# Performance work log

Measured on AMD Instinct MI355X. Metric: run time of the kernel, lower is better.

Reference implementation:

```python
import jax, jax.numpy as jnp
import numpy as np

B, V, D = 4096, 10000, 512
ANNEAL = 1.0
EPSILON = 1.0  # regularization_type = 'OT'


def setup_inputs() -> dict:
    key = jax.random.key(0)
    ks = jax.random.split(key, 8)
    return {
        "recon_x": jax.random.normal(ks[0], (B, V), dtype=jnp.float32),
        "logits_rec": jax.random.normal(ks[1], (B, V), dtype=jnp.float32),
        "logits_text": jax.random.normal(ks[2], (B, V), dtype=jnp.float32),
        "x": jax.random.uniform(ks[3], (B, V), dtype=jnp.float32),
        "mu": jax.random.normal(ks[4], (B, D), dtype=jnp.float32),
        "logvar": jax.random.normal(ks[5], (B, D), dtype=jnp.float32),
        "prior_mu": jax.random.normal(ks[6], (B, D), dtype=jnp.float32),
        "prior_logvar": jax.random.normal(ks[7], (B, D), dtype=jnp.float32),
    }


def _bce(logits, x):
    # -mean_b(mean_v(log_softmax(logits,1) * x)) == global mean since both
    # reductions are plain means over the full [B, V] tensor.
    return -jnp.mean(jax.nn.log_softmax(logits, axis=1) * x)


def _kld(m, lv):
    return -0.5 * jnp.mean(1.0 + lv - m * m - jnp.exp(lv))


def reference(recon_x, logits_rec, logits_text, x, mu, logvar, prior_mu, prior_logvar):
    BCE_merged = _bce(recon_x, x)
    BCE_text = _bce(logits_text, x)
    BCE_rec = _bce(logits_rec, x)
    BCE = (BCE_merged + BCE_text + BCE_rec) / 3.0

    KLD1 = _kld(mu, logvar)
    KLD2 = _kld(prior_mu, prior_logvar)

    # Bures-Wasserstein^2 between diagonal Gaussians. The torch code builds
    # dense diag matrices and runs batched Cholesky/bmm; for diagonal covs
    # L1 = diag(sqrt(s1)), L1 @ C2 @ L1^T = diag(s1*s2), chol -> diag(sqrt(s1*s2)),
    # so the math reduces exactly to the O(d) closed form below.
    s1 = jnp.exp(logvar)          # [B, D]
    s2 = jnp.exp(prior_logvar)    # [B, D]
    mean_dist_sq = jnp.sum((mu - prior_mu) ** 2, axis=1)            # [B]
    trace_term = jnp.sum(s1 + s2 - 2.0 * jnp.sqrt(s1 * s2), axis=1)  # [B]
    wasserstein_loss = jnp.mean(mean_dist_sq + trace_term)

    l = BCE + ANNEAL / 2.0 * (KLD1 + KLD2) + EPSILON * wasserstein_loss
    return (l, BCE, wasserstein_loss, BCE_rec, BCE_text, BCE_merged)
```

## Files before the change

### kernel.cpp

```cpp
#include <hip/hip_runtime.h>

#define NROWS 4096
#define NCOLS 10000
#define DDIM  512
#define NKLD  256

__device__ __forceinline__ float wave_reduce_sum(float v) {
    #pragma unroll
    for (int o = 32; o > 0; o >>= 1) v += __shfl_down(v, o, 64);
    return v;
}

__global__ __launch_bounds__(256) void fused_main_kernel(
    const float4* __restrict__ merged,
    const float4* __restrict__ rec,
    const float4* __restrict__ text,
    const float4* __restrict__ xr,
    const float4* __restrict__ mu, const float4* __restrict__ lv,
    const float4* __restrict__ pmu, const float4* __restrict__ plv,
    float* __restrict__ cm, float* __restrict__ ct, float* __restrict__ cr,
    float* __restrict__ k1o, float* __restrict__ k2o, float* __restrict__ wo)
{
    const int wave = threadIdx.x >> 6;
    const int lane = threadIdx.x & 63;

    if (blockIdx.x < NKLD) {
        const int nvec = NROWS * DDIM / 4;
        float k1 = 0.f, k2 = 0.f, wacc = 0.f;

        for (int i = blockIdx.x * 256 + threadIdx.x; i < nvec; i += NKLD * 256) {
            const float4 m  = mu[i];
            const float4 l  = lv[i];
            const float4 pm = pmu[i];
            const float4 pl = plv[i];

            #define KW_COMP(c)                                              \
            {                                                               \
                const float e1 = __expf(l.c);                               \
                const float e2 = __expf(pl.c);                              \
                k1 += 1.f + l.c - m.c * m.c - e1;                           \
                k2 += 1.f + pl.c - pm.c * pm.c - e2;                        \
                const float dm = m.c - pm.c;                                \
                wacc += dm * dm + e1 + e2 - 2.f * __expf(0.5f * (l.c + pl.c)); \
            }
            KW_COMP(x) KW_COMP(y) KW_COMP(z) KW_COMP(w)
            #undef KW_COMP
        }

        __shared__ float sm[4][3];
        k1 = wave_reduce_sum(k1);
        k2 = wave_reduce_sum(k2);
        wacc = wave_reduce_sum(wacc);
        if (lane == 0) { sm[wave][0] = k1; sm[wave][1] = k2; sm[wave][2] = wacc; }
        __syncthreads();
        if (threadIdx.x == 0) {
            k1o[blockIdx.x] = sm[0][0] + sm[1][0] + sm[2][0] + sm[3][0];
            k2o[blockIdx.x] = sm[0][1] + sm[1][1] + sm[2][1] + sm[3][1];
            wo[blockIdx.x]  = sm[0][2] + sm[1][2] + sm[2][2] + sm[3][2];
        }
        return;
    }

    const int row = blockIdx.x - NKLD;
    const int nvec = NCOLS / 4;
    const size_t base = (size_t)row * nvec;

    float se_m = 0.f, se_t = 0.f, se_r = 0.f;
    float d_m = 0.f, d_t = 0.f, d_r = 0.f;
    float sx = 0.f;

    #define BCE_BODY(xv, mv, tv, rv)                                          \
    {                                                                         \
        se_m += __expf(mv.x) + __expf(mv.y) + __expf(mv.z) + __expf(mv.w);    \
        se_t += __expf(tv.x) + __expf(tv.y) + __expf(tv.z) + __expf(tv.w);    \
        se_r += __expf(rv.x) + __expf(rv.y) + __expf(rv.z) + __expf(rv.w);    \
        d_m += mv.x * xv.x + mv.y * xv.y + mv.z * xv.z + mv.w * xv.w;         \
        d_t += tv.x * xv.x + tv.y * xv.y + tv.z * xv.z + tv.w * xv.w;         \
        d_r += rv.x * xv.x + rv.y * xv.y + rv.z * xv.z + rv.w * xv.w;         \
        sx  += xv.x + xv.y + xv.z + xv.w;                                     \
    }

    int i = threadIdx.x;
    for (; i + 256 < nvec; i += 512) {
        const float4 xv0 = xr[base + i];
        const float4 mv0 = merged[base + i];
        const float4 tv0 = text[base + i];
        const float4 rv0 = rec[base + i];
        const float4 xv1 = xr[base + i + 256];
        const float4 mv1 = merged[base + i + 256];
        const float4 tv1 = text[base + i + 256];
        const float4 rv1 = rec[base + i + 256];
        BCE_BODY(xv0, mv0, tv0, rv0)
        BCE_BODY(xv1, mv1, tv1, rv1)
    }
    for (; i < nvec; i += 256) {
        const float4 xv = xr[base + i];
        const float4 mv = merged[base + i];
        const float4 tv = text[base + i];
        const float4 rv = rec[base + i];
        BCE_BODY(xv, mv, tv, rv)
    }
    #undef BCE_BODY

    __shared__ float sm2[4][7];
    float vals[7] = {se_m, se_t, se_r, d_m, d_t, d_r, sx};
    #pragma unroll
    for (int k = 0; k < 7; ++k) vals[k] = wave_reduce_sum(vals[k]);
    if (lane == 0) {
        #pragma unroll
        for (int k = 0; k < 7; ++k) sm2[wave][k] = vals[k];
    }
    __syncthreads();

    if (threadIdx.x == 0) {
        float t[7];
        #pragma unroll
        for (int k = 0; k < 7; ++k)
            t[k] = sm2[0][k] + sm2[1][k] + sm2[2][k] + sm2[3][k];
        const float sumx = t[6];
        cm[row] = t[3] - __logf(t[0]) * sumx;
        ct[row] = t[4] - __logf(t[1]) * sumx;
        cr[row] = t[5] - __logf(t[2]) * sumx;
    }
}

__global__ __launch_bounds__(256) void finalize_kernel(
    const float* __restrict__ cm, const float* __restrict__ ct,
    const float* __restrict__ cr, const float* __restrict__ k1p,
    const float* __restrict__ k2p, const float* __restrict__ wp,
    float* __restrict__ out)
{
    float sm_ = 0.f, st_ = 0.f, sr_ = 0.f;
    for (int i = threadIdx.x; i < NROWS; i += 256) {
        sm_ += cm[i]; st_ += ct[i]; sr_ += cr[i];
    }
    float s1 = 0.f, s2 = 0.f, sw = 0.f;
    for (int i = threadIdx.x; i < NKLD; i += 256) {
        s1 += k1p[i]; s2 += k2p[i]; sw += wp[i];
    }

    __shared__ float sh[4][6];
    float vals[6] = {sm_, st_, sr_, s1, s2, sw};
    #pragma unroll
    for (int k = 0; k < 6; ++k) vals[k] = wave_reduce_sum(vals[k]);
    const int wave = threadIdx.x >> 6;
    const int lane = threadIdx.x & 63;
    if (lane == 0) {
        #pragma unroll
        for (int k = 0; k < 6; ++k) sh[wave][k] = vals[k];
    }
    __syncthreads();

    if (threadIdx.x == 0) {
        float t[6];
        #pragma unroll
        for (int k = 0; k < 6; ++k)
            t[k] = sh[0][k] + sh[1][k] + sh[2][k] + sh[3][k];

        const float invBV = 1.f / ((float)NROWS * (float)NCOLS);
        const float BCE_merged = -t[0] * invBV;
        const float BCE_text   = -t[1] * invBV;
        const float BCE_rec    = -t[2] * invBV;
        const float BCE = (BCE_merged + BCE_text + BCE_rec) * (1.f / 3.f);

        const float invBD = 1.f / ((float)NROWS * (float)DDIM);
        const float KLD1 = -0.5f * t[3] * invBD;
        const float KLD2 = -0.5f * t[4] * invBD;
        const float wass = t[5] / (float)NROWS;

        const float l = BCE + 0.5f * (KLD1 + KLD2) + wass;

        out[0] = l;
        out[1] = BCE;
        out[2] = wass;
        out[3] = BCE_rec;
        out[4] = BCE_text;
        out[5] = BCE_merged;
    }
}

extern "C" void kernel_launch(void* const* d_in, const int* in_sizes, int n_in,
                              void* d_out, int out_size, void* d_ws, size_t ws_size,
                              hipStream_t stream) {
    const float4* recon_x      = (const float4*)d_in[0];
    const float4* logits_rec   = (const float4*)d_in[1];
    const float4* logits_text  = (const float4*)d_in[2];
    const float4* x            = (const float4*)d_in[3];
    const float4* mu           = (const float4*)d_in[4];
    const float4* logvar       = (const float4*)d_in[5];
    const float4* prior_mu     = (const float4*)d_in[6];
    const float4* prior_logvar = (const float4*)d_in[7];

    float* ws = (float*)d_ws;
    float* cm = ws;
    float* ct = ws + NROWS;
    float* cr = ws + 2 * NROWS;
    float* k1p = ws + 3 * NROWS;
    float* k2p = ws + 3 * NROWS + NKLD;
    float* wp  = ws + 3 * NROWS + 2 * NKLD;

    hipLaunchKernelGGL(fused_main_kernel, dim3(NKLD + NROWS), dim3(256), 0, stream,
                       recon_x, logits_rec, logits_text, x,
                       mu, logvar, prior_mu, prior_logvar,
                       cm, ct, cr, k1p, k2p, wp);
    hipLaunchKernelGGL(finalize_kernel, dim3(1), dim3(256), 0, stream,
                       cm, ct, cr, k1p, k2p, wp, (float*)d_out);
}
```

Before: 128.9 us.

## Merge KLD/Wasserstein work into BCE row blocks, two rows per block

Removes the separate group of KLD blocks and hands each of 2048 blocks one float4 slice of the latent tensors plus two BCE rows, so every block is uniform. The BCE loop is unrolled three-deep instead of two to keep more loads in flight. The finalize kernel now reduces 2048 partials per quantity. Each block gets longer and there is an extra sync between rows, and the grid is smaller, which changes tail behaviour.

```diff
diff --git a/kernel.cpp b/kernel.cpp
--- a/kernel.cpp
+++ b/kernel.cpp
@@ -3,7 +3,7 @@
 #define NROWS 4096
 #define NCOLS 10000
 #define DDIM  512
-#define NKLD  256
+#define NBLK  2048
 
 __device__ __forceinline__ float wave_reduce_sum(float v) {
     #pragma unroll
@@ -24,103 +24,115 @@
     const int wave = threadIdx.x >> 6;
     const int lane = threadIdx.x & 63;
 
-    if (blockIdx.x < NKLD) {
-        const int nvec = NROWS * DDIM / 4;
-        float k1 = 0.f, k2 = 0.f, wacc = 0.f;
-
-        for (int i = blockIdx.x * 256 + threadIdx.x; i < nvec; i += NKLD * 256) {
-            const float4 m  = mu[i];
-            const float4 l  = lv[i];
-            const float4 pm = pmu[i];
-            const float4 pl = plv[i];
-
-            #define KW_COMP(c)                                              \
-            {                                                               \
-                const float e1 = __expf(l.c);                               \
-                const float e2 = __expf(pl.c);                              \
-                k1 += 1.f + l.c - m.c * m.c - e1;                           \
-                k2 += 1.f + pl.c - pm.c * pm.c - e2;                        \
-                const float dm = m.c - pm.c;                                \
-                wacc += dm * dm + e1 + e2 - 2.f * __expf(0.5f * (l.c + pl.c)); \
-            }
-            KW_COMP(x) KW_COMP(y) KW_COMP(z) KW_COMP(w)
-            #undef KW_COMP
-        }
-
-        __shared__ float sm[4][3];
+    float k1 = 0.f, k2 = 0.f, wacc = 0.f;
+    {
+        const int i = blockIdx.x * 256 + threadIdx.x;
+        const float4 m  = mu[i];
+        const float4 l  = lv[i];
+        const float4 pm = pmu[i];
+        const float4 pl = plv[i];
+        #pragma unroll
+        for (int c = 0; c < 4; ++c) {
+            const float lc  = ((const float*)&l)[c];
+            const float plc = ((const float*)&pl)[c];
+            const float mc  = ((const float*)&m)[c];
+            const float pmc = ((const float*)&pm)[c];
+            const float e1 = __expf(lc);
+            const float e2 = __expf(plc);
+            k1 += 1.f + lc - mc * mc - e1;
+            k2 += 1.f + plc - pmc * pmc - e2;
+            const float dm = mc - pmc;
+            wacc += dm * dm + e1 + e2 - 2.f * __expf(0.5f * (lc + plc));
+        }
+    }
+
+    const int nvec = NCOLS / 4;
+    float acc_m = 0.f, acc_t = 0.f, acc_r = 0.f;
+    __shared__ float sm2[4][7];
+
+    #pragma unroll
+    for (int half = 0; half < 2; ++half) {
+        const int row = blockIdx.x * 2 + half;
+        const size_t base = (size_t)row * nvec;
+
+        float se_m = 0.f, se_t = 0.f, se_r = 0.f;
+        float d_m = 0.f, d_t = 0.f, d_r = 0.f;
+        float sx = 0.f;
+
+        #define BCE_BODY(xv, mv, tv, rv)                                          \
+        {                                                                         \
+            se_m += __expf(mv.x) + __expf(mv.y) + __expf(mv.z) + __expf(mv.w);    \
+            se_t += __expf(tv.x) + __expf(tv.y) + __expf(tv.z) + __expf(tv.w);    \
+            se_r += __expf(rv.x) + __expf(rv.y) + __expf(rv.z) + __expf(rv.w);    \
+            d_m += mv.x * xv.x + mv.y * xv.y + mv.z * xv.z + mv.w * xv.w;         \
+            d_t += tv.x * xv.x + tv.y * xv.y + tv.z * xv.z + tv.w * xv.w;         \
+            d_r += rv.x * xv.x + rv.y * xv.y + rv.z * xv.z + rv.w * xv.w;         \
+            sx  += xv.x + xv.y + xv.z + xv.w;                                     \
+        }
+
+        int i = threadIdx.x;
+        for (; i + 512 < nvec; i += 768) {
+            const float4 xv0 = xr[base + i];
+            const float4 xv1 = xr[base + i + 256];
+            const float4 xv2 = xr[base + i + 512];
+            const float4 mv0 = merged[base + i];
+            const float4 mv1 = merged[base + i + 256];
+            const float4 mv2 = merged[base + i + 512];
+            const float4 tv0 = text[base + i];
+            const float4 tv1 = text[base + i + 256];
+            const float4 tv2 = text[base + i + 512];
+            const float4 rv0 = rec[base + i];
+            const float4 rv1 = rec[base + i + 256];
+            const float4 rv2 = rec[base + i + 512];
+            BCE_BODY(xv0, mv0, tv0, rv0)
+            BCE_BODY(xv1, mv1, tv1, rv1)
+            BCE_BODY(xv2, mv2, tv2, rv2)
+        }
+        for (; i < nvec; i += 256) {
+            const float4 xv = xr[base + i];
+            const float4 mv = merged[base + i];
+            const float4 tv = text[base + i];
+            const float4 rv = rec[base + i];
+            BCE_BODY(xv, mv, tv, rv)
+        }
+        #undef BCE_BODY
+
+        float vals[7] = {se_m, se_t, se_r, d_m, d_t, d_r, sx};
+        #pragma unroll
+        for (int k = 0; k < 7; ++k) vals[k] = wave_reduce_sum(vals[k]);
+        if (lane == 0) {
+            #pragma unroll
+            for (int k = 0; k < 7; ++k) sm2[wave][k] = vals[k];
+        }
+        __syncthreads();
+        if (threadIdx.x == 0) {
+            float t[7];
+            #pragma unroll
+            for (int k = 0; k < 7; ++k)
+                t[k] = sm2[0][k] + sm2[1][k] + sm2[2][k] + sm2[3][k];
+            const float sumx = t[6];
+            acc_m += t[3] - __logf(t[0]) * sumx;
+            acc_t += t[4] - __logf(t[1]) * sumx;
+            acc_r += t[5] - __logf(t[2]) * sumx;
+        }
+        __syncthreads();
+    }
+
+    {
+        __shared__ float smk[4][3];
         k1 = wave_reduce_sum(k1);
         k2 = wave_reduce_sum(k2);
         wacc = wave_reduce_sum(wacc);
-        if (lane == 0) { sm[wave][0] = k1; sm[wave][1] = k2; sm[wave][2] = wacc; }
+        if (lane == 0) { smk[wave][0] = k1; smk[wave][1] = k2; smk[wave][2] = wacc; }
         __syncthreads();
         if (threadIdx.x == 0) {
-            k1o[blockIdx.x] = sm[0][0] + sm[1][0] + sm[2][0] + sm[3][0];
-            k2o[blockIdx.x] = sm[0][1] + sm[1][1] + sm[2][1] + sm[3][1];
-            wo[blockIdx.x]  = sm[0][2] + sm[1][2] + sm[2][2] + sm[3][2];
-        }
-        return;
-    }
-
-    const int row = blockIdx.x - NKLD;
-    const int nvec = NCOLS / 4;
-    const size_t base = (size_t)row * nvec;
-
-    float se_m = 0.f, se_t = 0.f, se_r = 0.f;
-    float d_m = 0.f, d_t = 0.f, d_r = 0.f;
-    float sx = 0.f;
-
-    #define BCE_BODY(xv, mv, tv, rv)                                          \
-    {                                                                         \
-        se_m += __expf(mv.x) + __expf(mv.y) + __expf(mv.z) + __expf(mv.w);    \
-        se_t += __expf(tv.x) + __expf(tv.y) + __expf(tv.z) + __expf(tv.w);    \
-        se_r += __expf(rv.x) + __expf(rv.y) + __expf(rv.z) + __expf(rv.w);    \
-        d_m += mv.x * xv.x + mv.y * xv.y + mv.z * xv.z + mv.w * xv.w;         \
-        d_t += tv.x * xv.x + tv.y * xv.y + tv.z * xv.z + tv.w * xv.w;         \
-        d_r += rv.x * xv.x + rv.y * xv.y + rv.z * xv.z + rv.w * xv.w;         \
-        sx  += xv.x + xv.y + xv.z + xv.w;                                     \
-    }
-
-    int i = threadIdx.x;
-    for (; i + 256 < nvec; i += 512) {
-        const float4 xv0 = xr[base + i];
-        const float4 mv0 = merged[base + i];
-        const float4 tv0 = text[base + i];
-        const float4 rv0 = rec[base + i];
-        const float4 xv1 = xr[base + i + 256];
-        const float4 mv1 = merged[base + i + 256];
-        const float4 tv1 = text[base + i + 256];
-        const float4 rv1 = rec[base + i + 256];
-        BCE_BODY(xv0, mv0, tv0, rv0)
-        BCE_BODY(xv1, mv1, tv1, rv1)
-    }
-    for (; i < nvec; i += 256) {
-        const float4 xv = xr[base + i];
-        const float4 mv = merged[base + i];
-        const float4 tv = text[base + i];
-        const float4 rv = rec[base + i];
-        BCE_BODY(xv, mv, tv, rv)
-    }
-    #undef BCE_BODY
-
-    __shared__ float sm2[4][7];
-    float vals[7] = {se_m, se_t, se_r, d_m, d_t, d_r, sx};
-    #pragma unroll
-    for (int k = 0; k < 7; ++k) vals[k] = wave_reduce_sum(vals[k]);
-    if (lane == 0) {
-        #pragma unroll
-        for (int k = 0; k < 7; ++k) sm2[wave][k] = vals[k];
-    }
-    __syncthreads();
-
-    if (threadIdx.x == 0) {
-        float t[7];
-        #pragma unroll
-        for (int k = 0; k < 7; ++k)
-            t[k] = sm2[0][k] + sm2[1][k] + sm2[2][k] + sm2[3][k];
-        const float sumx = t[6];
-        cm[row] = t[3] - __logf(t[0]) * sumx;
-        ct[row] = t[4] - __logf(t[1]) * sumx;
-        cr[row] = t[5] - __logf(t[2]) * sumx;
+            k1o[blockIdx.x] = smk[0][0] + smk[1][0] + smk[2][0] + smk[3][0];
+            k2o[blockIdx.x] = smk[0][1] + smk[1][1] + smk[2][1] + smk[3][1];
+            wo[blockIdx.x]  = smk[0][2] + smk[1][2] + smk[2][2] + smk[3][2];
+            cm[blockIdx.x] = acc_m;
+            ct[blockIdx.x] = acc_t;
+            cr[blockIdx.x] = acc_r;
+        }
     }
 }
 
@@ -130,24 +142,20 @@
     const float* __restrict__ k2p, const float* __restrict__ wp,
     float* __restrict__ out)
 {
-    float sm_ = 0.f, st_ = 0.f, sr_ = 0.f;
-    for (int i = threadIdx.x; i < NROWS; i += 256) {
-        sm_ += cm[i]; st_ += ct[i]; sr_ += cr[i];
-    }
-    float s1 = 0.f, s2 = 0.f, sw = 0.f;
-    for (int i = threadIdx.x; i < NKLD; i += 256) {
-        s1 += k1p[i]; s2 += k2p[i]; sw += wp[i];
+    float v[6] = {0.f, 0.f, 0.f, 0.f, 0.f, 0.f};
+    for (int i = threadIdx.x; i < NBLK; i += 256) {
+        v[0] += cm[i]; v[1] += ct[i]; v[2] += cr[i];
+        v[3] += k1p[i]; v[4] += k2p[i]; v[5] += wp[i];
     }
 
     __shared__ float sh[4][6];
-    float vals[6] = {sm_, st_, sr_, s1, s2, sw};
     #pragma unroll
-    for (int k = 0; k < 6; ++k) vals[k] = wave_reduce_sum(vals[k]);
+    for (int k = 0; k < 6; ++k) v[k] = wave_reduce_sum(v[k]);
     const int wave = threadIdx.x >> 6;
     const int lane = threadIdx.x & 63;
     if (lane == 0) {
         #pragma unroll
-        for (int k = 0; k < 6; ++k) sh[wave][k] = vals[k];
+        for (int k = 0; k < 6; ++k) sh[wave][k] = v[k];
     }
     __syncthreads();
 
@@ -187,19 +195,19 @@
     const float4* logits_text  = (const float4*)d_in[2];
     const float4* x            = (const float4*)d_in[3];
     const float4* mu           = (const float4*)d_in[4];
-    const float4* logvar       = (const float4*)d_in[5];
+    const float4* logvar      = (const float4*)d_in[5];
     const float4* prior_mu     = (const float4*)d_in[6];
     const float4* prior_logvar = (const float4*)d_in[7];
 
     float* ws = (float*)d_ws;
-    float* cm = ws;
-    float* ct = ws + NROWS;
-    float* cr = ws + 2 * NROWS;
-    float* k1p = ws + 3 * NROWS;
-    float* k2p = ws + 3 * NROWS + NKLD;
-    float* wp  = ws + 3 * NROWS + 2 * NKLD;
-
-    hipLaunchKernelGGL(fused_main_kernel, dim3(NKLD + NROWS), dim3(256), 0, stream,
+    float* cm  = ws;
+    float* ct  = ws + NBLK;
+    float* cr  = ws + 2 * NBLK;
+    float* k1p = ws + 3 * NBLK;
+    float* k2p = ws + 4 * NBLK;
+    float* wp  = ws + 5 * NBLK;
+
+    hipLaunchKernelGGL(fused_main_kernel, dim3(NBLK), dim3(256), 0, stream,
                        recon_x, logits_rec, logits_text, x,
                        mu, logvar, prior_mu, prior_logvar,
                        cm, ct, cr, k1p, k2p, wp);
```

Measured after the change: 127.1 us. About the same (-1.4%).
